# Performance work log

Hardware: AMD Instinct MI355X
Metric: run time of the kernel (lower is better)

The kernel has to match this reference:

```python
import jax, jax.numpy as jnp
import numpy as np

B, S, DM, DE, H, DH, DC, DCq, DR = 4, 2048, 1024, 1024, 16, 64, 128, 128, 32
SCALE = 1.0 / np.sqrt(DH + DR)


def _rope_tables(seq_len, dim, theta=10000.0):
    inv = 1.0 / (theta ** (jnp.arange(0, dim, 2, dtype=jnp.float32) / dim))  # [dim/2]
    t = jnp.arange(seq_len, dtype=jnp.float32)
    ang = t[:, None] * inv[None, :]  # [S, dim/2]
    return jnp.cos(ang), jnp.sin(ang)


def _apply_rope(xq, xk, cos, sin):
    # xq, xk: [B, S, H, DR]; complex rotary on (even, odd) pairs
    def rot(x):
        s = x.shape
        xr = x.reshape(*s[:-1], s[-1] // 2, 2)
        r, i = xr[..., 0], xr[..., 1]
        c = cos[None, :s[1], None, :]
        sn = sin[None, :s[1], None, :]
        out = jnp.stack([r * c - i * sn, r * sn + i * c], axis=-1)
        return out.reshape(s)
    return rot(xq), rot(xk)


def setup_inputs() -> dict:
    key = jax.random.key(0)
    ks = jax.random.split(key, 10)
    def lin(k, din, dout):
        return 0.02 * jax.random.normal(k, (din, dout), jnp.float32)
    inp = {
        "x": jax.random.normal(ks[0], (B, S, DM), jnp.float32),
        "mask": jnp.tril(jnp.ones((S, S), jnp.float32))[None, None],
        "W_dkv": lin(ks[1], DM, DC),  "b_dkv": jnp.zeros((DC,), jnp.float32),
        "W_dq":  lin(ks[2], DM, DCq), "b_dq":  jnp.zeros((DCq,), jnp.float32),
        "W_uk":  lin(ks[3], DC, DE),  "b_uk":  jnp.zeros((DE,), jnp.float32),
        "W_uv":  lin(ks[4], DC, DE),  "b_uv":  jnp.zeros((DE,), jnp.float32),
        "W_uq":  lin(ks[5], DCq, DE), "b_uq":  jnp.zeros((DE,), jnp.float32),
        "W_qr":  lin(ks[6], DCq, DR * H), "b_qr": jnp.zeros((DR * H,), jnp.float32),
        "W_kr":  lin(ks[7], DM, DR),  "b_kr": jnp.zeros((DR,), jnp.float32),
        "W_o":   lin(ks[8], DE, DM),  "b_o":  jnp.zeros((DM,), jnp.float32),
    }
    return inp


def reference(x, mask, W_dkv, b_dkv, W_dq, b_dq, W_uk, b_uk, W_uv, b_uv,
              W_uq, b_uq, W_qr, b_qr, W_kr, b_kr, W_o, b_o):
    bs, seq_len, _ = x.shape
    cos, sin = _rope_tables(2 * S, DR)

    c_q = x @ W_dq + b_dq            # [B,S,DCq]
    c_kv = x @ W_dkv + b_dkv         # [B,S,DC]
    k_r = x @ W_kr + b_kr            # [B,S,DR]

    q_c = (c_q @ W_uq + b_uq).reshape(bs, seq_len, H, DH)
    k_c = (c_kv @ W_uk + b_uk).reshape(bs, seq_len, H, DH)
    v_c = (c_kv @ W_uv + b_uv).reshape(bs, seq_len, H, DH)

    q_r = (c_q @ W_qr + b_qr).reshape(bs, seq_len, H, DR)
    k_r = jnp.broadcast_to(k_r[:, :, None, :], (bs, seq_len, H, DR))
    q_r, k_r = _apply_rope(q_r, k_r, cos, sin)

    q_t = jnp.concatenate([q_c, q_r], axis=-1)  # [B,S,H,DH+DR]
    k_t = jnp.concatenate([k_c, k_r], axis=-1)

    attn = jnp.einsum('bqhd,bkhd->bhqk', q_t, k_t) * SCALE  # [B,H,S,S]
    m = jnp.where(mask == 0, -jnp.inf, mask)  # faithful masked_fill then add
    attn = attn + m
    p = jax.nn.softmax(attn, axis=-1)
    out = jnp.einsum('bhqk,bkhd->bqhd', p, v_c).reshape(bs, seq_len, H * DH)
    return out @ W_o + b_o
```

## Files before the change

kernel.cpp:

```cpp
#include <hip/hip_runtime.h>
#include <cstdint>
#include <cstddef>

#define S_ 2048
#define B_ 4
#define H_ 16
#define ALPHA_Q 0.14724394f

typedef __attribute__((ext_vector_type(8))) __bf16 bf16x8;
typedef __attribute__((ext_vector_type(4))) __bf16 bf16x4;
typedef __attribute__((ext_vector_type(4))) float f32x4;
typedef __attribute__((ext_vector_type(16))) float f32x16;

__device__ __forceinline__ f32x16 mfma32(bf16x8 a, bf16x8 b, f32x16 c) {
  return __builtin_amdgcn_mfma_f32_32x32x16_bf16(a, b, c, 0, 0, 0);
}

__device__ __forceinline__ void gll16(const void* g, void* l) {
  __builtin_amdgcn_global_load_lds(
      (__attribute__((address_space(1))) void*)(uintptr_t)g,
      (__attribute__((address_space(3))) void*)(uint32_t)(uintptr_t)l,
      16, 0, 0);
}

__device__ __forceinline__ int cvtpk(float lo, float hi) {
  int r;
  asm("v_cvt_pk_bf16_f32 %0, %1, %2" : "=v"(r) : "v"(lo), "v"(hi));
  return r;
}

union PAU { int w[4]; bf16x8 v; };

__device__ __forceinline__ bf16x8 packPA(int hi, float a0, float a1, float a2,
                                         float a3, float b0, float b1, float b2,
                                         float b3) {
  const int Ylo = cvtpk(a0, a1);
  const int Yhi = cvtpk(a2, a3);
  const int Xlo = cvtpk(b0, b1);
  const int Xhi = cvtpk(b2, b3);
  const int t0 = __shfl_xor(hi ? Ylo : Xlo, 32);
  const int t1 = __shfl_xor(hi ? Yhi : Xhi, 32);
  PAU u;
  u.w[0] = hi ? t0 : Ylo;
  u.w[1] = hi ? t1 : Yhi;
  u.w[2] = hi ? Xlo : t0;
  u.w[3] = hi ? Xhi : t1;
  return u.v;
}

__device__ __forceinline__ float tmax16(const f32x16& v) {
  float a[8];
#pragma unroll
  for (int i = 0; i < 8; ++i) a[i] = fmaxf(v[i], v[i + 8]);
#pragma unroll
  for (int s = 4; s > 0; s >>= 1)
#pragma unroll
    for (int i = 0; i < s; ++i) a[i] = fmaxf(a[i], a[i + s]);
  return a[0];
}

__global__ __launch_bounds__(256) void mla_prep(
    const float* __restrict__ x, __bf16* __restrict__ xb,
    const float* __restrict__ W_dq, const float* __restrict__ W_dkv,
    const float* __restrict__ W_kr, const float* __restrict__ W_uq,
    const float* __restrict__ W_qr, const float* __restrict__ W_uk,
    const float* __restrict__ W_uv, const float* __restrict__ W_o,
    __bf16* __restrict__ WdT, __bf16* __restrict__ WuqT,
    __bf16* __restrict__ WukvT, __bf16* __restrict__ WoT,
    const float* __restrict__ b_dq, const float* __restrict__ b_dkv,
    const float* __restrict__ b_kr, const float* __restrict__ b_uq,
    const float* __restrict__ b_qr, const float* __restrict__ b_uk,
    const float* __restrict__ b_uv, float* __restrict__ bias_d,
    float* __restrict__ bias_uq, float* __restrict__ bias_ukv,
    float* __restrict__ ropec, float* __restrict__ ropes) {
  const int id = blockIdx.x;
  const int t = threadIdx.x;
  __shared__ float tile[32][33];

  if (id < 4096) {
    const size_t i = ((size_t)id * 256 + t) * 8;
    float4 a = *(const float4*)&x[i];
    float4 b = *(const float4*)&x[i + 4];
    bf16x8 v;
    v[0] = (__bf16)a.x; v[1] = (__bf16)a.y; v[2] = (__bf16)a.z; v[3] = (__bf16)a.w;
    v[4] = (__bf16)b.x; v[5] = (__bf16)b.y; v[6] = (__bf16)b.z; v[7] = (__bf16)b.w;
    *(bf16x8*)&xb[i] = v;
    return;
  }
  if (id < 5856) {
    int rel = id - 4096;
    const float* W;
    __bf16* WT;
    int K, N, nt;
    if (rel < 128)      { W = W_dq;  WT = WdT;                      K = 1024; N = 128;  nt = 4; }
    else if (rel < 256) { W = W_dkv; WT = WdT + (size_t)128 * 1024; K = 1024; N = 128;  nt = 4;  rel -= 128; }
    else if (rel < 288) { W = W_kr;  WT = WdT + (size_t)256 * 1024; K = 1024; N = 32;   nt = 1;  rel -= 256; }
    else if (rel < 416) { W = W_uq;  WT = WuqT;                     K = 128;  N = 1024; nt = 32; rel -= 288; }
    else if (rel < 480) { W = W_qr;  WT = WuqT + (size_t)1024 * 128; K = 128; N = 512;  nt = 16; rel -= 416; }
    else if (rel < 608) { W = W_uk;  WT = WukvT;                    K = 128;  N = 1024; nt = 32; rel -= 480; }
    else if (rel < 736) { W = W_uv;  WT = WukvT + (size_t)1024 * 128; K = 128; N = 1024; nt = 32; rel -= 608; }
    else                { W = W_o;   WT = WoT;                      K = 1024; N = 1024; nt = 32; rel -= 736; }
    const int n0 = (rel % nt) * 32, k0 = (rel / nt) * 32;
    const int tx = t & 31, ty = t >> 5;
#pragma unroll
    for (int i = 0; i < 32; i += 8)
      tile[ty + i][tx] = W[(size_t)(k0 + ty + i) * N + n0 + tx];
    __syncthreads();
#pragma unroll
    for (int i = 0; i < 32; i += 8)
      WT[(size_t)(n0 + ty + i) * K + k0 + tx] = (__bf16)tile[tx][ty + i];
    return;
  }
  if (id < 5984) {
    const int g = (id - 5856) * 256 + t;
    const int s = g >> 4, i = g & 15;
    const float inv = exp2f(-(float)i * (13.287712379549449f / 16.0f));
    const float ang = (float)s * inv;
    ropec[g] = cosf(ang);
    ropes[g] = sinf(ang);
    return;
  }
  {
    const int g = (id - 5984) * 256 + t;
    if (g < 384)
      bias_d[g] = (g < 128) ? b_dq[g] : (g < 256) ? b_dkv[g - 128]
                 : (g < 288) ? b_kr[g - 256] : 0.f;
    if (g < 1536) bias_uq[g] = (g < 1024) ? b_uq[g] : b_qr[g - 1024];
    if (g < 2048) bias_ukv[g] = (g < 1024) ? b_uk[g] : b_uv[g - 1024];
  }
}

template <int MODE>
__global__ __launch_bounds__(256) void gemm32(
    const __bf16* __restrict__ A, int lda, const __bf16* __restrict__ BT, int ldbt,
    const float* __restrict__ bias, void* __restrict__ C0, int ldc, int K) {
  const int n0 = blockIdx.x * 128;
  const int m0 = blockIdx.y * 128;
  const int wave = threadIdx.x >> 6, lane = threadIdx.x & 63;
  const int hi = lane >> 5, lq = lane & 31;
  const int wm = (wave >> 1) * 64, wn = (wave & 1) * 64;
  __shared__ __bf16 __attribute__((aligned(16))) ldsA[8 * 128 * 8];
  __shared__ __bf16 __attribute__((aligned(16))) ldsB[8 * 128 * 8];

  const f32x16 fz16 = {0.f, 0.f, 0.f, 0.f, 0.f, 0.f, 0.f, 0.f,
                       0.f, 0.f, 0.f, 0.f, 0.f, 0.f, 0.f, 0.f};
  f32x16 acc00 = fz16, acc01 = fz16, acc10 = fz16, acc11 = fz16;

  for (int k0 = 0; k0 < K; k0 += 64) {
    __syncthreads();
#pragma unroll
    for (int i = 0; i < 8; ++i) {
      const int c = wave * 8 + i;
      if (c < 16) {
        const int sl = c >> 1, half = c & 1;
        gll16(&A[(size_t)(m0 + half * 64 + lane) * lda + k0 + sl * 8],
              &ldsA[(sl * 128 + half * 64) * 8]);
      } else {
        const int cc = c - 16;
        const int sl = cc >> 1, half = cc & 1;
        gll16(&BT[(size_t)(n0 + half * 64 + lane) * ldbt + k0 + sl * 8],
              &ldsB[(sl * 128 + half * 64) * 8]);
      }
    }
    __syncthreads();

#pragma unroll
    for (int ks = 0; ks < 4; ++ks) {
      const int sl = ks * 2 + hi;
      bf16x8 a0 = *(const bf16x8*)&ldsA[(sl * 128 + wm + lq) * 8];
      bf16x8 a1 = *(const bf16x8*)&ldsA[(sl * 128 + wm + 32 + lq) * 8];
      bf16x8 b0 = *(const bf16x8*)&ldsB[(sl * 128 + wn + lq) * 8];
      bf16x8 b1 = *(const bf16x8*)&ldsB[(sl * 128 + wn + 32 + lq) * 8];
      acc00 = mfma32(a0, b0, acc00);
      acc01 = mfma32(a0, b1, acc01);
      acc10 = mfma32(a1, b0, acc10);
      acc11 = mfma32(a1, b1, acc11);
    }
  }

  const f32x16* accs[2][2] = {{&acc00, &acc01}, {&acc10, &acc11}};
#pragma unroll
  for (int ni = 0; ni < 2; ++ni) {
    const int col = n0 + wn + ni * 32 + lq;
    const float bv = bias[col];
#pragma unroll
    for (int mi = 0; mi < 2; ++mi) {
      const f32x16& ac = *accs[mi][ni];
#pragma unroll
      for (int r = 0; r < 16; ++r) {
        const int row = m0 + wm + mi * 32 + (r & 3) + 8 * (r >> 2) + 4 * hi;
        const float v = ac[r] + bv;
        if (MODE == 0)
          ((__bf16*)C0)[(size_t)row * ldc + col] = (__bf16)v;
        else
          ((float*)C0)[(size_t)row * ldc + col] = v;
      }
    }
  }
}

__global__ __launch_bounds__(256) void gemm32up(
    const __bf16* __restrict__ cqkvr, const __bf16* __restrict__ WuqT,
    const __bf16* __restrict__ WukvT, const float* __restrict__ bias_uq,
    const float* __restrict__ bias_ukv, __bf16* __restrict__ qt,
    __bf16* __restrict__ qr, __bf16* __restrict__ ktb, __bf16* __restrict__ vv) {
  const bool isQ = blockIdx.x < 12;
  const int n0 = (isQ ? blockIdx.x : (blockIdx.x - 12)) * 128;
  const __bf16* A = cqkvr + (isQ ? 0 : 128);
  const __bf16* BT = isQ ? WuqT : WukvT;
  const float* bias = isQ ? bias_uq : bias_ukv;
  const int m0 = blockIdx.y * 128;
  const int wave = threadIdx.x >> 6, lane = threadIdx.x & 63;
  const int hi = lane >> 5, lq = lane & 31;
  const int wm = (wave >> 1) * 64, wn = (wave & 1) * 64;
  __shared__ __bf16 __attribute__((aligned(16))) ldsA[8 * 128 * 8];
  __shared__ __bf16 __attribute__((aligned(16))) ldsB[8 * 128 * 8];

  const f32x16 fz16 = {0.f, 0.f, 0.f, 0.f, 0.f, 0.f, 0.f, 0.f,
                       0.f, 0.f, 0.f, 0.f, 0.f, 0.f, 0.f, 0.f};
  f32x16 acc00 = fz16, acc01 = fz16, acc10 = fz16, acc11 = fz16;

  for (int k0 = 0; k0 < 128; k0 += 64) {
    __syncthreads();
#pragma unroll
    for (int i = 0; i < 8; ++i) {
      const int c = wave * 8 + i;
      if (c < 16) {
        const int sl = c >> 1, half = c & 1;
        gll16(&A[(size_t)(m0 + half * 64 + lane) * 384 + k0 + sl * 8],
              &ldsA[(sl * 128 + half * 64) * 8]);
      } else {
        const int cc = c - 16;
        const int sl = cc >> 1, half = cc & 1;
        gll16(&BT[(size_t)(n0 + half * 64 + lane) * 128 + k0 + sl * 8],
              &ldsB[(sl * 128 + half * 64) * 8]);
      }
    }
    __syncthreads();

#pragma unroll
    for (int ks = 0; ks < 4; ++ks) {
      const int sl = ks * 2 + hi;
      bf16x8 a0 = *(const bf16x8*)&ldsA[(sl * 128 + wm + lq) * 8];
      bf16x8 a1 = *(const bf16x8*)&ldsA[(sl * 128 + wm + 32 + lq) * 8];
      bf16x8 b0 = *(const bf16x8*)&ldsB[(sl * 128 + wn + lq) * 8];
      bf16x8 b1 = *(const bf16x8*)&ldsB[(sl * 128 + wn + 32 + lq) * 8];
      acc00 = mfma32(a0, b0, acc00);
      acc01 = mfma32(a0, b1, acc01);
      acc10 = mfma32(a1, b0, acc10);
      acc11 = mfma32(a1, b1, acc11);
    }
  }

  const f32x16* accs[2][2] = {{&acc00, &acc01}, {&acc10, &acc11}};
#pragma unroll
  for (int ni = 0; ni < 2; ++ni) {
    const int col = n0 + wn + ni * 32 + lq;
    const float bv = bias[col];
#pragma unroll
    for (int mi = 0; mi < 2; ++mi) {
      const f32x16& ac = *accs[mi][ni];
#pragma unroll
      for (int r = 0; r < 16; ++r) {
        const int row = m0 + wm + mi * 32 + (r & 3) + 8 * (r >> 2) + 4 * hi;
        const float v = ac[r] + bv;
        const int b = row >> 11, s = row & 2047;
        if (col < 1024) {
          const int h = col >> 6, d = col & 63;
          const size_t o = ((size_t)(b * H_ + h) * S_ + s) * 96 + d;
          if (isQ)
            qt[o] = (__bf16)(v * ALPHA_Q);
          else
            ktb[o] = (__bf16)v;
        } else {
          if (isQ)
            qr[(size_t)row * 512 + col - 1024] = (__bf16)v;
          else
            vv[(size_t)row * 1024 + col - 1024] = (__bf16)v;
        }
      }
    }
  }
}

__global__ __launch_bounds__(256) void mla_glue(
    const __bf16* __restrict__ qr, const __bf16* __restrict__ cqkvr,
    const float* __restrict__ ropec, const float* __restrict__ ropes,
    __bf16* __restrict__ qt, __bf16* __restrict__ ktb,
    const __bf16* __restrict__ vv, __bf16* __restrict__ vt) {
  __shared__ __bf16 __attribute__((aligned(16))) tile[64][72];
  const int t = threadIdx.x;
  if (blockIdx.x < 8192) {
    const int gid = blockIdx.x * 256 + t;
    const int bs = gid >> 8;
    const int h = (gid >> 4) & 15;
    const int i = gid & 15;
    const int b = bs >> 11, s = bs & 2047;
    const float c = ropec[s * 16 + i], sn = ropes[s * 16 + i];
    const size_t o = ((size_t)(b * H_ + h) * S_ + s) * 96 + 64 + 2 * i;
    {
      const float r = (float)qr[(size_t)bs * 512 + h * 32 + 2 * i];
      const float im = (float)qr[(size_t)bs * 512 + h * 32 + 2 * i + 1];
      qt[o] = (__bf16)((r * c - im * sn) * ALPHA_Q);
      qt[o + 1] = (__bf16)((r * sn + im * c) * ALPHA_Q);
    }
    {
      const float r = (float)cqkvr[(size_t)bs * 384 + 256 + 2 * i];
      const float im = (float)cqkvr[(size_t)bs * 384 + 256 + 2 * i + 1];
      ktb[o] = (__bf16)(r * c - im * sn);
      ktb[o + 1] = (__bf16)(r * sn + im * c);
    }
    return;
  }
  const int bid = blockIdx.x - 8192;
  const int s0 = (bid & 31) * 64;
  const int bh = bid >> 5;
  const int b = bh >> 4, h = bh & 15;
  {
    const int r = t >> 2, c0 = (t & 3) * 16;
    const size_t src = (size_t)(b * S_ + s0 + r) * 1024 + h * 64 + c0;
    bf16x8 u0 = *(const bf16x8*)&vv[src];
    bf16x8 u1 = *(const bf16x8*)&vv[src + 8];
    *(bf16x8*)&tile[r][c0] = u0;
    *(bf16x8*)&tile[r][c0 + 8] = u1;
  }
  __syncthreads();
  {
    const int d = t >> 2, sc0 = (t & 3) * 16;
    bf16x8 w0, w1;
#pragma unroll
    for (int e = 0; e < 8; ++e) {
      w0[e] = tile[sc0 + e][d];
      w1[e] = tile[sc0 + 8 + e][d];
    }
    const size_t dst = ((size_t)bh * 64 + d) * S_ + s0 + sc0;
    *(bf16x8*)&vt[dst] = w0;
    *(bf16x8*)&vt[dst + 8] = w1;
  }
}

__global__ __launch_bounds__(256, 3) void mla_attn(const __bf16* __restrict__ qt,
                                                   const __bf16* __restrict__ kt,
                                                   const __bf16* __restrict__ vt,
                                                   __bf16* __restrict__ ao) {
  const int bh = blockIdx.x;
  const int j = blockIdx.y;
  const int wave = threadIdx.x >> 6, lane = threadIdx.x & 63;
  const int hi = lane >> 5, lq = lane & 31;
  const __bf16* Q = qt + (size_t)bh * S_ * 96;
  const __bf16* Kp = kt + (size_t)bh * S_ * 96;
  const __bf16* Vp = vt + (size_t)bh * 64 * S_;
  const int bb = bh >> 4, h = bh & 15;

  __shared__ __bf16 __attribute__((aligned(16))) kbuf[2][12 * 512];
  __shared__ __bf16 __attribute__((aligned(16))) vbuf[2][8 * 512];

  const f32x16 fz16 = {0.f, 0.f, 0.f, 0.f, 0.f, 0.f, 0.f, 0.f,
                       0.f, 0.f, 0.f, 0.f, 0.f, 0.f, 0.f, 0.f};
  bf16x8 onesA;
#pragma unroll
  for (int e = 0; e < 8; ++e) onesA[e] = (__bf16)1.0f;

  for (int pass = 0; pass < 2; ++pass) {
    const int qblk = pass ? (15 - j) : j;
    const int q0w = qblk * 128 + wave * 32;

    bf16x8 qf[6];
#pragma unroll
    for (int kd = 0; kd < 6; ++kd)
      qf[kd] = *(const bf16x8*)&Q[(size_t)(q0w + lq) * 96 + kd * 16 + hi * 8];

    f32x16 o0 = fz16, o1 = fz16, Lacc = fz16;
    float m = -3.0e38f;

    const int tEnd = (q0w + 31) >> 6;
    const int tMax = qblk * 2 + 1;

    const __bf16* gsrc[5];
#pragma unroll
    for (int i = 0; i < 5; ++i) {
      const int c = wave + 4 * i;
      gsrc[i] = (c < 12) ? Kp + (size_t)lane * 96 + c * 8
                         : Vp + (size_t)lane * S_ + (c - 12) * 8;
    }
    auto stage = [&](int bsel) {
#pragma unroll
      for (int i = 0; i < 5; ++i) {
        const int c = wave + 4 * i;
        if (c < 12) {
          gll16(gsrc[i], &kbuf[bsel][c * 512]);
          gsrc[i] += 64 * 96;
        } else {
          gll16(gsrc[i], &vbuf[bsel][(c - 12) * 512]);
          gsrc[i] += 64;
        }
      }
    };

    stage(0);
    __syncthreads();

    int bsel = 0;
    for (int t = 0; t <= tMax; ++t) {
      if (t < tMax) stage(bsel ^ 1);
      if (t <= tEnd) {
        f32x16 s0 = fz16, s1 = fz16;
#pragma unroll
        for (int kd = 0; kd < 6; ++kd) {
          const int sl = kd * 2 + hi;
          bf16x8 a0 = *(const bf16x8*)&kbuf[bsel][(sl * 64 + lq) * 8];
          bf16x8 a1 = *(const bf16x8*)&kbuf[bsel][(sl * 64 + 32 + lq) * 8];
          s0 = mfma32(a0, qf[kd], s0);
          s1 = mfma32(a1, qf[kd], s1);
        }
        if (t == tEnd) {
          const int qg = q0w + lq;
          const int kvb = t * 64 + 4 * hi;
#pragma unroll
          for (int r = 0; r < 16; ++r) {
            const int crow = (r & 3) + 8 * (r >> 2);
            if (kvb + crow > qg) s0[r] = -3.0e38f;
            if (kvb + 32 + crow > qg) s1[r] = -3.0e38f;
          }
        }
        float tm = fmaxf(tmax16(s0), tmax16(s1));
        tm = fmaxf(tm, __shfl_xor(tm, 32));
        if (!__all(tm <= m + 8.0f)) {
          const float mnew = fmaxf(m, tm);
          const float sc = exp2f(m - mnew);
          m = mnew;
          Lacc[0] *= sc;
          o0 *= sc;
          o1 *= sc;
        }
        float p0[16], p1[16];
#pragma unroll
        for (int r = 0; r < 16; ++r) {
          p0[r] = exp2f(s0[r] - m);
          p1[r] = exp2f(s1[r] - m);
        }
        bf16x8 pa[4];
        pa[0] = packPA(hi, p0[0], p0[1], p0[2], p0[3], p0[4], p0[5], p0[6], p0[7]);
        pa[1] = packPA(hi, p0[8], p0[9], p0[10], p0[11], p0[12], p0[13], p0[14], p0[15]);
        pa[2] = packPA(hi, p1[0], p1[1], p1[2], p1[3], p1[4], p1[5], p1[6], p1[7]);
        pa[3] = packPA(hi, p1[8], p1[9], p1[10], p1[11], p1[12], p1[13], p1[14], p1[15]);
#pragma unroll
        for (int ks = 0; ks < 4; ++ks) {
          const int sl = ks * 2 + hi;
          bf16x8 v0 = *(const bf16x8*)&vbuf[bsel][(sl * 64 + lq) * 8];
          bf16x8 v1 = *(const bf16x8*)&vbuf[bsel][(sl * 64 + 32 + lq) * 8];
          o0 = mfma32(v0, pa[ks], o0);
          o1 = mfma32(v1, pa[ks], o1);
          Lacc = mfma32(onesA, pa[ks], Lacc);
        }
      }
      __syncthreads();
      bsel ^= 1;
    }

    const float invL = 1.0f / Lacc[0];
    __bf16* aorow = ao + (size_t)(bb * S_ + q0w + lq) * 1024 + h * 64;
#pragma unroll
    for (int rr = 0; rr < 4; ++rr) {
      bf16x4 w0, w1;
#pragma unroll
      for (int jj = 0; jj < 4; ++jj) {
        w0[jj] = (__bf16)(o0[4 * rr + jj] * invL);
        w1[jj] = (__bf16)(o1[4 * rr + jj] * invL);
      }
      *(bf16x4*)&aorow[rr * 8 + 4 * hi] = w0;
      *(bf16x4*)&aorow[32 + rr * 8 + 4 * hi] = w1;
    }
  }
}

extern "C" void kernel_launch(void* const* d_in, const int* in_sizes, int n_in,
                              void* d_out, int out_size, void* d_ws, size_t ws_size,
                              hipStream_t stream) {
  (void)in_sizes; (void)n_in; (void)out_size; (void)ws_size;
  const float* x = (const float*)d_in[0];
  const float* W_dkv = (const float*)d_in[2];
  const float* b_dkv = (const float*)d_in[3];
  const float* W_dq = (const float*)d_in[4];
  const float* b_dq = (const float*)d_in[5];
  const float* W_uk = (const float*)d_in[6];
  const float* b_uk = (const float*)d_in[7];
  const float* W_uv = (const float*)d_in[8];
  const float* b_uv = (const float*)d_in[9];
  const float* W_uq = (const float*)d_in[10];
  const float* b_uq = (const float*)d_in[11];
  const float* W_qr = (const float*)d_in[12];
  const float* b_qr = (const float*)d_in[13];
  const float* W_kr = (const float*)d_in[14];
  const float* b_kr = (const float*)d_in[15];
  const float* W_o = (const float*)d_in[16];
  const float* b_o = (const float*)d_in[17];
  float* out = (float*)d_out;

  char* ws = (char*)d_ws;
  size_t off = 0;
  auto take = [&](size_t nbytes) -> char* {
    char* p = ws + off;
    off += (nbytes + 255) & ~(size_t)255;
    return p;
  };
  __bf16* xb = (__bf16*)take((size_t)8192 * 1024 * 2);
  __bf16* WdT = (__bf16*)take((size_t)384 * 1024 * 2);
  __bf16* WuqT = (__bf16*)take((size_t)1536 * 128 * 2);
  __bf16* WukvT = (__bf16*)take((size_t)2048 * 128 * 2);
  __bf16* WoT = (__bf16*)take((size_t)1024 * 1024 * 2);
  float* bias_d = (float*)take(384 * 4);
  float* bias_uq = (float*)take(1536 * 4);
  float* bias_ukv = (float*)take(2048 * 4);
  float* ropec = (float*)take((size_t)S_ * 16 * 4);
  float* ropes = (float*)take((size_t)S_ * 16 * 4);
  __bf16* cqkvr = (__bf16*)take((size_t)8192 * 384 * 2);
  __bf16* qr = (__bf16*)take((size_t)8192 * 512 * 2);
  __bf16* vv = (__bf16*)take((size_t)8192 * 1024 * 2);
  __bf16* qt = (__bf16*)take((size_t)B_ * H_ * S_ * 96 * 2);
  __bf16* ktb = (__bf16*)take((size_t)B_ * H_ * S_ * 96 * 2);
  __bf16* vt = (__bf16*)take((size_t)B_ * H_ * 64 * S_ * 2);
  __bf16* aout = (__bf16*)take((size_t)8192 * 1024 * 2);

  hipMemsetAsync(WdT + (size_t)288 * 1024, 0, (size_t)96 * 1024 * 2, stream);

  mla_prep<<<6000, 256, 0, stream>>>(x, xb, W_dq, W_dkv, W_kr, W_uq, W_qr, W_uk,
                                     W_uv, W_o, WdT, WuqT, WukvT, WoT, b_dq,
                                     b_dkv, b_kr, b_uq, b_qr, b_uk, b_uv, bias_d,
                                     bias_uq, bias_ukv, ropec, ropes);

  gemm32<0><<<dim3(3, 64), 256, 0, stream>>>(xb, 1024, WdT, 1024, bias_d,
                                             cqkvr, 384, 1024);
  gemm32up<<<dim3(28, 64), 256, 0, stream>>>(cqkvr, WuqT, WukvT, bias_uq,
                                             bias_ukv, qt, qr, ktb, vv);

  mla_glue<<<8192 + 2048, 256, 0, stream>>>(qr, cqkvr, ropec, ropes, qt, ktb, vv, vt);

  mla_attn<<<dim3(64, 8), 256, 0, stream>>>(qt, ktb, vt, aout);

  gemm32<1><<<dim3(8, 64), 256, 0, stream>>>(aout, 1024, WoT, 1024, b_o, out,
                                             1024, 1024);
}
```

Before: 339.9 us.

## Process paired causal query blocks in one KV sweep sharing staged tiles

Instead of two sequential passes, each loading K/V for a different query block (j and 15-j), the kernel now keeps both query blocks' fragments and accumulators live and processes them in a single sweep over KV tiles. Each staged K/V tile is reused by both blocks, which roughly halves the global-to-LDS traffic and the barrier count for the short block. The doubled register state forces launch bounds down from 3 to 2 blocks per SM, lowering occupancy and risking spills.

```diff
diff --git a/kernel.cpp b/kernel.cpp
--- a/kernel.cpp
+++ b/kernel.cpp
@@ -339,7 +339,7 @@
   }
 }
 
-__global__ __launch_bounds__(256, 3) void mla_attn(const __bf16* __restrict__ qt,
+__global__ __launch_bounds__(256, 2) void mla_attn(const __bf16* __restrict__ qt,
                                                    const __bf16* __restrict__ kt,
                                                    const __bf16* __restrict__ vt,
                                                    __bf16* __restrict__ ao) {
@@ -361,103 +361,113 @@
 #pragma unroll
   for (int e = 0; e < 8; ++e) onesA[e] = (__bf16)1.0f;
 
-  for (int pass = 0; pass < 2; ++pass) {
-    const int qblk = pass ? (15 - j) : j;
-    const int q0w = qblk * 128 + wave * 32;
-
-    bf16x8 qf[6];
-#pragma unroll
-    for (int kd = 0; kd < 6; ++kd)
-      qf[kd] = *(const bf16x8*)&Q[(size_t)(q0w + lq) * 96 + kd * 16 + hi * 8];
-
-    f32x16 o0 = fz16, o1 = fz16, Lacc = fz16;
-    float m = -3.0e38f;
-
-    const int tEnd = (q0w + 31) >> 6;
-    const int tMax = qblk * 2 + 1;
-
-    const __bf16* gsrc[5];
+  const int qblkA = j, qblkB = 15 - j;
+  const int q0wA = qblkA * 128 + wave * 32;
+  const int q0wB = qblkB * 128 + wave * 32;
+
+  bf16x8 qfA[6], qfB[6];
+#pragma unroll
+  for (int kd = 0; kd < 6; ++kd) {
+    qfA[kd] = *(const bf16x8*)&Q[(size_t)(q0wA + lq) * 96 + kd * 16 + hi * 8];
+    qfB[kd] = *(const bf16x8*)&Q[(size_t)(q0wB + lq) * 96 + kd * 16 + hi * 8];
+  }
+
+  f32x16 o0A = fz16, o1A = fz16, LA = fz16;
+  f32x16 o0B = fz16, o1B = fz16, LB = fz16;
+  float mA = -3.0e38f, mB = -3.0e38f;
+
+  const int tEndA = (q0wA + 31) >> 6;
+  const int tEndB = (q0wB + 31) >> 6;
+  const int tMax = qblkB * 2 + 1;
+
+  const __bf16* gsrc[5];
+#pragma unroll
+  for (int i = 0; i < 5; ++i) {
+    const int c = wave + 4 * i;
+    gsrc[i] = (c < 12) ? Kp + (size_t)lane * 96 + c * 8
+                       : Vp + (size_t)lane * S_ + (c - 12) * 8;
+  }
+  auto stage = [&](int bsel) {
 #pragma unroll
     for (int i = 0; i < 5; ++i) {
       const int c = wave + 4 * i;
-      gsrc[i] = (c < 12) ? Kp + (size_t)lane * 96 + c * 8
-                         : Vp + (size_t)lane * S_ + (c - 12) * 8;
-    }
-    auto stage = [&](int bsel) {
-#pragma unroll
-      for (int i = 0; i < 5; ++i) {
-        const int c = wave + 4 * i;
-        if (c < 12) {
-          gll16(gsrc[i], &kbuf[bsel][c * 512]);
-          gsrc[i] += 64 * 96;
-        } else {
-          gll16(gsrc[i], &vbuf[bsel][(c - 12) * 512]);
-          gsrc[i] += 64;
-        }
-      }
-    };
-
-    stage(0);
+      if (c < 12) {
+        gll16(gsrc[i], &kbuf[bsel][c * 512]);
+        gsrc[i] += 64 * 96;
+      } else {
+        gll16(gsrc[i], &vbuf[bsel][(c - 12) * 512]);
+        gsrc[i] += 64;
+      }
+    }
+  };
+
+  auto process = [&](const bf16x8* qf, f32x16& o0, f32x16& o1, f32x16& Lacc,
+                     float& m, int q0w, int tEnd, int t, int bsel) {
+    f32x16 s0 = fz16, s1 = fz16;
+#pragma unroll
+    for (int kd = 0; kd < 6; ++kd) {
+      const int sl = kd * 2 + hi;
+      bf16x8 a0 = *(const bf16x8*)&kbuf[bsel][(sl * 64 + lq) * 8];
+      bf16x8 a1 = *(const bf16x8*)&kbuf[bsel][(sl * 64 + 32 + lq) * 8];
+      s0 = mfma32(a0, qf[kd], s0);
+      s1 = mfma32(a1, qf[kd], s1);
+    }
+    if (t == tEnd) {
+      const int qg = q0w + lq;
+      const int kvb = t * 64 + 4 * hi;
+#pragma unroll
+      for (int r = 0; r < 16; ++r) {
+        const int crow = (r & 3) + 8 * (r >> 2);
+        if (kvb + crow > qg) s0[r] = -3.0e38f;
+        if (kvb + 32 + crow > qg) s1[r] = -3.0e38f;
+      }
+    }
+    float tm = fmaxf(tmax16(s0), tmax16(s1));
+    tm = fmaxf(tm, __shfl_xor(tm, 32));
+    if (!__all(tm <= m + 8.0f)) {
+      const float mnew = fmaxf(m, tm);
+      const float sc = exp2f(m - mnew);
+      m = mnew;
+      Lacc[0] *= sc;
+      o0 *= sc;
+      o1 *= sc;
+    }
+    float p0[16], p1[16];
+#pragma unroll
+    for (int r = 0; r < 16; ++r) {
+      p0[r] = exp2f(s0[r] - m);
+      p1[r] = exp2f(s1[r] - m);
+    }
+    bf16x8 pa[4];
+    pa[0] = packPA(hi, p0[0], p0[1], p0[2], p0[3], p0[4], p0[5], p0[6], p0[7]);
+    pa[1] = packPA(hi, p0[8], p0[9], p0[10], p0[11], p0[12], p0[13], p0[14], p0[15]);
+    pa[2] = packPA(hi, p1[0], p1[1], p1[2], p1[3], p1[4], p1[5], p1[6], p1[7]);
+    pa[3] = packPA(hi, p1[8], p1[9], p1[10], p1[11], p1[12], p1[13], p1[14], p1[15]);
+#pragma unroll
+    for (int ks = 0; ks < 4; ++ks) {
+      const int sl = ks * 2 + hi;
+      bf16x8 v0 = *(const bf16x8*)&vbuf[bsel][(sl * 64 + lq) * 8];
+      bf16x8 v1 = *(const bf16x8*)&vbuf[bsel][(sl * 64 + 32 + lq) * 8];
+      o0 = mfma32(v0, pa[ks], o0);
+      o1 = mfma32(v1, pa[ks], o1);
+      Lacc = mfma32(onesA, pa[ks], Lacc);
+    }
+  };
+
+  stage(0);
+  __syncthreads();
+
+  int bsel = 0;
+  for (int t = 0; t <= tMax; ++t) {
+    if (t < tMax) stage(bsel ^ 1);
+    if (t <= tEndA) process(qfA, o0A, o1A, LA, mA, q0wA, tEndA, t, bsel);
+    if (t <= tEndB) process(qfB, o0B, o1B, LB, mB, q0wB, tEndB, t, bsel);
     __syncthreads();
-
-    int bsel = 0;
-    for (int t = 0; t <= tMax; ++t) {
-      if (t < tMax) stage(bsel ^ 1);
-      if (t <= tEnd) {
-        f32x16 s0 = fz16, s1 = fz16;
-#pragma unroll
-        for (int kd = 0; kd < 6; ++kd) {
-          const int sl = kd * 2 + hi;
-          bf16x8 a0 = *(const bf16x8*)&kbuf[bsel][(sl * 64 + lq) * 8];
-          bf16x8 a1 = *(const bf16x8*)&kbuf[bsel][(sl * 64 + 32 + lq) * 8];
-          s0 = mfma32(a0, qf[kd], s0);
-          s1 = mfma32(a1, qf[kd], s1);
-        }
-        if (t == tEnd) {
-          const int qg = q0w + lq;
-          const int kvb = t * 64 + 4 * hi;
-#pragma unroll
-          for (int r = 0; r < 16; ++r) {
-            const int crow = (r & 3) + 8 * (r >> 2);
-            if (kvb + crow > qg) s0[r] = -3.0e38f;
-            if (kvb + 32 + crow > qg) s1[r] = -3.0e38f;
-          }
-        }
-        float tm = fmaxf(tmax16(s0), tmax16(s1));
-        tm = fmaxf(tm, __shfl_xor(tm, 32));
-        if (!__all(tm <= m + 8.0f)) {
-          const float mnew = fmaxf(m, tm);
-          const float sc = exp2f(m - mnew);
-          m = mnew;
-          Lacc[0] *= sc;
-          o0 *= sc;
-          o1 *= sc;
-        }
-        float p0[16], p1[16];
-#pragma unroll
-        for (int r = 0; r < 16; ++r) {
-          p0[r] = exp2f(s0[r] - m);
-          p1[r] = exp2f(s1[r] - m);
-        }
-        bf16x8 pa[4];
-        pa[0] = packPA(hi, p0[0], p0[1], p0[2], p0[3], p0[4], p0[5], p0[6], p0[7]);
-        pa[1] = packPA(hi, p0[8], p0[9], p0[10], p0[11], p0[12], p0[13], p0[14], p0[15]);
-        pa[2] = packPA(hi, p1[0], p1[1], p1[2], p1[3], p1[4], p1[5], p1[6], p1[7]);
-        pa[3] = packPA(hi, p1[8], p1[9], p1[10], p1[11], p1[12], p1[13], p1[14], p1[15]);
-#pragma unroll
-        for (int ks = 0; ks < 4; ++ks) {
-          const int sl = ks * 2 + hi;
-          bf16x8 v0 = *(const bf16x8*)&vbuf[bsel][(sl * 64 + lq) * 8];
-          bf16x8 v1 = *(const bf16x8*)&vbuf[bsel][(sl * 64 + 32 + lq) * 8];
-          o0 = mfma32(v0, pa[ks], o0);
-          o1 = mfma32(v1, pa[ks], o1);
-          Lacc = mfma32(onesA, pa[ks], Lacc);
-        }
-      }
-      __syncthreads();
-      bsel ^= 1;
-    }
-
+    bsel ^= 1;
+  }
+
+  auto writeOut = [&](const f32x16& o0, const f32x16& o1, const f32x16& Lacc,
+                      int q0w) {
     const float invL = 1.0f / Lacc[0];
     __bf16* aorow = ao + (size_t)(bb * S_ + q0w + lq) * 1024 + h * 64;
 #pragma unroll
@@ -471,7 +481,9 @@
       *(bf16x4*)&aorow[rr * 8 + 4 * hi] = w0;
       *(bf16x4*)&aorow[32 + rr * 8 + 4 * hi] = w1;
     }
-  }
+  };
+  writeOut(o0A, o1A, LA, q0wA);
+  writeOut(o0B, o1B, LB, q0wB);
 }
 
 extern "C" void kernel_launch(void* const* d_in, const int* in_sizes, int n_in,
```

Measured after the change: 336.6 us. Within noise of the previous version (-0.9%).
